# Kernel tuning notes

Hardware: AMD Instinct MI355X
Metric: run time of the kernel (lower is better)

The kernel has to match this reference:

```python
import jax, jax.numpy as jnp
import numpy as np

EPS = 1e-5
GROUPS = 32

def group_norm(x, gamma, beta):
    B, C, H, W = x.shape
    g = x.reshape(B, GROUPS, C // GROUPS, H, W)
    mu = g.mean(axis=(2, 3, 4), keepdims=True)
    var = g.var(axis=(2, 3, 4), keepdims=True)
    g = (g - mu) * jax.lax.rsqrt(var + EPS)
    x = g.reshape(B, C, H, W)
    return x * gamma[None, :, None, None] + beta[None, :, None, None]

def setup_inputs() -> dict:
    key = jax.random.key(0)
    ks = jax.random.split(key, 6)
    C = 512
    x = jax.random.normal(ks[0], (16, C, 32, 32), dtype=jnp.float32)
    gamma = jnp.ones((C,), jnp.float32)
    beta = jnp.zeros((C,), jnp.float32)
    w_qkv = jax.random.normal(ks[1], (3 * C, C), jnp.float32) / np.sqrt(C)
    b_qkv = jnp.zeros((3 * C,), jnp.float32)
    w_proj = jax.random.normal(ks[2], (C, C), jnp.float32) / np.sqrt(C)
    b_proj = jnp.zeros((C,), jnp.float32)
    return {"x": x, "gamma": gamma, "beta": beta, "w_qkv": w_qkv,
            "b_qkv": b_qkv, "w_proj": w_proj, "b_proj": b_proj}

def reference(x, gamma, beta, w_qkv, b_qkv, w_proj, b_proj):
    B, C, H, W = x.shape
    h = group_norm(x, gamma, beta)
    # 1x1 conv == per-pixel linear over channels
    qkv = jnp.einsum('bchw,oc->bohw', h, w_qkv) + b_qkv[None, :, None, None]
    q, k, v = jnp.split(qkv, 3, axis=1)
    N = H * W
    q = q.reshape(B, C, N)            # [B,C,N]
    k = k.reshape(B, C, N)
    v = v.reshape(B, C, N)
    attn = jnp.einsum('bci,bcj->bij', q, k) / jnp.sqrt(jnp.float32(C))
    attn = jax.nn.softmax(attn, axis=-1)          # [B,N,N]
    out = jnp.einsum('bij,bcj->bci', attn, v)     # [B,C,N]
    out = out.reshape(B, C, H, W)
    out = jnp.einsum('bchw,oc->bohw', out, w_proj) + b_proj[None, :, None, None]
    return x + out
```

## Files before the change

kernel.cpp:

```cpp
#include <hip/hip_runtime.h>
#include <hip/hip_bf16.h>

#define BATCH 16
#define CH    512
#define NPIX  1024
#define GRP   32
#define CPG   16

typedef __attribute__((ext_vector_type(8))) short bf16x8;
typedef __attribute__((ext_vector_type(4))) float f32x4;

__device__ __forceinline__ ushort f2b(float f) {
    union { float f; unsigned u; } v; v.f = f;
    unsigned u = v.u;
    u += 0x7FFF + ((u >> 16) & 1);
    return (ushort)(u >> 16);
}

#define GLD16(gp, lp) __builtin_amdgcn_global_load_lds( \
    (__attribute__((address_space(1))) void*)(gp), \
    (__attribute__((address_space(3))) void*)(lp), 16, 0, 0)

__global__ __launch_bounds__(256) void convert_weights(
    const float* __restrict__ wq, const float* __restrict__ wp,
    ushort* __restrict__ wq_b, ushort* __restrict__ wp_b,
    float* __restrict__ rowsum) {
    int i = blockIdx.x * 256 + threadIdx.x;
    if (i < 786432) wq_b[i] = f2b(wq[i]);
    else            wp_b[i - 786432] = f2b(wp[i - 786432]);
    if (i < BATCH * NPIX) rowsum[i] = 0.f;
}

__global__ __launch_bounds__(256) void gn_fused(
    const float* __restrict__ x, const float* __restrict__ gamma,
    const float* __restrict__ beta, ushort* __restrict__ hT) {
    __shared__ float xs[CPG * NPIX];
    __shared__ float as[4], bs[4];
    int g = blockIdx.x, b = blockIdx.y;
    const float4* p = (const float4*)(x + ((size_t)b * CH + g * CPG) * NPIX);
    float4* xs4 = (float4*)xs;
    float s = 0.f, ss = 0.f;
    for (int i = threadIdx.x; i < 4096; i += 256) {
        float4 v = p[i];
        xs4[i] = v;
        s  += v.x + v.y + v.z + v.w;
        ss += v.x*v.x + v.y*v.y + v.z*v.z + v.w*v.w;
    }
    for (int o = 1; o < 64; o <<= 1) { s += __shfl_xor(s, o); ss += __shfl_xor(ss, o); }
    int w = threadIdx.x >> 6;
    if ((threadIdx.x & 63) == 0) { as[w] = s; bs[w] = ss; }
    __syncthreads();
    s  = as[0] + as[1] + as[2] + as[3];
    ss = bs[0] + bs[1] + bs[2] + bs[3];
    float m   = s * (1.0f / 16384.0f);
    float var = ss * (1.0f / 16384.0f) - m * m;
    float r   = rsqrtf(var + 1e-5f);

    int c0 = g * CPG;
    float ga[CPG], be[CPG];
#pragma unroll
    for (int c = 0; c < CPG; c++) {
        float gg = gamma[c0 + c] * r;
        ga[c] = gg;
        be[c] = beta[c0 + c] - m * gg;
    }
    ushort tmp[CPG];
#pragma unroll
    for (int i = 0; i < 4; i++) {
        int n = threadIdx.x + i * 256;
#pragma unroll
        for (int c = 0; c < CPG; c++)
            tmp[c] = f2b(xs[c * NPIX + n] * ga[c] + be[c]);
        uint4* dst = (uint4*)(hT + ((size_t)b * NPIX + n) * CH + c0);
        dst[0] = *(const uint4*)&tmp[0];
        dst[1] = *(const uint4*)&tmp[8];
    }
}

#define BK 64

template<int EPI, int BMt, int BNt>
__global__ __launch_bounds__(256, 4) void gemm_bt(
    const ushort* __restrict__ A, long sA, int lda,
    const ushort* __restrict__ Bt, long sB, int ldb,
    int K,
    void* __restrict__ Out, long sO, int ldo,
    const float* __restrict__ bias,
    const float* __restrict__ resid,
    ushort* __restrict__ vout,
    float* __restrict__ rowsum,
    float scale) {
    constexpr int FM = BMt / 32;
    constexpr int FN = BNt / 32;
    constexpr int SA = BMt / 32;
    constexpr int SB = BNt / 32;
    __shared__ __align__(16) ushort sh[(BMt + BNt) * BK];
    ushort* As = sh;
    ushort* Bs = sh + BMt * BK;

    int nx = gridDim.x, ny = gridDim.y;
    int L = blockIdx.x + nx * (blockIdx.y + ny * blockIdx.z);
    int per = (nx * ny * (int)gridDim.z) >> 3;
    int wid = (L & 7) * per + (L >> 3);
    int bx = wid % nx; wid /= nx;
    int by = wid % ny;
    int b  = wid / ny;

    A  += (size_t)b * sA;
    Bt += (size_t)b * sB;
    int m0 = by * BMt, n0 = bx * BNt;
    int tid = threadIdx.x;
    int lane = tid & 63;
    int wave = tid >> 6;
    int q = lane >> 4, l = lane & 15;
    int wm = (wave >> 1) * (BMt / 2), wn = (wave & 1) * (BNt / 2);

    int aoff[SA], boff[SB], lofa[SA], lofb[SB];
#pragma unroll
    for (int i = 0; i < SA; i++) {
        int p = tid + i * 256, r = p >> 3, g = (p & 7) ^ (r & 7);
        aoff[i] = (m0 + r) * lda + g * 8;
        lofa[i] = p * 8;
    }
#pragma unroll
    for (int i = 0; i < SB; i++) {
        int p = tid + i * 256, r = p >> 3, g = (p & 7) ^ (r & 7);
        boff[i] = (n0 + r) * ldb + g * 8;
        lofb[i] = p * 8;
    }

    int offA[FM][2], offB[FN][2];
#pragma unroll
    for (int mi = 0; mi < FM; mi++) {
        int r = wm + mi * 16 + l;
#pragma unroll
        for (int kk = 0; kk < 2; kk++)
            offA[mi][kk] = r * 64 + ((((kk << 2) | q) ^ (r & 7)) * 8);
    }
#pragma unroll
    for (int ni = 0; ni < FN; ni++) {
        int r = wn + ni * 16 + l;
#pragma unroll
        for (int kk = 0; kk < 2; kk++)
            offB[ni][kk] = r * 64 + ((((kk << 2) | q) ^ (r & 7)) * 8);
    }

    f32x4 zero = {0.f, 0.f, 0.f, 0.f};
    f32x4 acc[FM][FN];
#pragma unroll
    for (int mi = 0; mi < FM; mi++)
#pragma unroll
        for (int ni = 0; ni < FN; ni++) acc[mi][ni] = zero;

    for (int k0 = 0; k0 < K; k0 += BK) {
        __syncthreads();
#pragma unroll
        for (int i = 0; i < SA; i++) GLD16(A + aoff[i] + k0, As + lofa[i]);
#pragma unroll
        for (int i = 0; i < SB; i++) GLD16(Bt + boff[i] + k0, Bs + lofb[i]);
        __syncthreads();
#pragma unroll
        for (int kk = 0; kk < 2; kk++) {
            bf16x8 af[FM], bfr[FN];
#pragma unroll
            for (int mi = 0; mi < FM; mi++) af[mi]  = *(const bf16x8*)(As + offA[mi][kk]);
#pragma unroll
            for (int ni = 0; ni < FN; ni++) bfr[ni] = *(const bf16x8*)(Bs + offB[ni][kk]);
#pragma unroll
            for (int mi = 0; mi < FM; mi++)
#pragma unroll
                for (int ni = 0; ni < FN; ni++)
                    acc[mi][ni] = __builtin_amdgcn_mfma_f32_16x16x32_bf16(
                        af[mi], bfr[ni], acc[mi][ni], 0, 0, 0);
        }
    }

    if (EPI == 0) {
        if (n0 >= 1024) {
            __syncthreads();
#pragma unroll
            for (int mi = 0; mi < FM; mi++)
#pragma unroll
                for (int ni = 0; ni < FN; ni++) {
                    int nl = wn + ni * 16 + l;
                    float bi = bias[n0 + nl];
#pragma unroll
                    for (int rg = 0; rg < 4; rg++) {
                        int ml = wm + mi * 16 + q * 4 + rg;
                        int pos = (ml >> 3) ^ (nl & 15);
                        sh[nl * 128 + pos * 8 + (ml & 7)] = f2b(acc[mi][ni][rg] + bi);
                    }
                }
            __syncthreads();
#pragma unroll
            for (int i = 0; i < 8; i++) {
                int idx = tid + i * 256;
                int nl = idx >> 4, ch = idx & 15;
                int g2 = ch ^ (nl & 15);
                uint4 val = *(const uint4*)&sh[nl * 128 + g2 * 8];
                *(uint4*)(vout + (size_t)b * (512 * 1024)
                          + (size_t)(n0 - 1024 + nl) * 1024 + m0 + ch * 8) = val;
            }
            return;
        }
#pragma unroll
        for (int mi = 0; mi < FM; mi++)
#pragma unroll
            for (int ni = 0; ni < FN; ni++) {
                int n = n0 + wn + ni * 16 + l;
                float bi = bias[n];
#pragma unroll
                for (int rg = 0; rg < 4; rg++) {
                    int m = m0 + wm + mi * 16 + q * 4 + rg;
                    ((ushort*)Out)[(size_t)b * sO + (size_t)m * ldo + n] =
                        f2b(acc[mi][ni][rg] + bi);
                }
            }
        return;
    }
    if (EPI == 1) {
#pragma unroll
        for (int mi = 0; mi < FM; mi++) {
            float rsum[4] = {0.f, 0.f, 0.f, 0.f};
#pragma unroll
            for (int ni = 0; ni < FN; ni++) {
                int n = n0 + wn + ni * 16 + l;
#pragma unroll
                for (int rg = 0; rg < 4; rg++) {
                    int m = m0 + wm + mi * 16 + q * 4 + rg;
                    float u = __expf(acc[mi][ni][rg] * scale);
                    rsum[rg] += u;
                    ((ushort*)Out)[(size_t)b * sO + (size_t)m * ldo + n] = f2b(u);
                }
            }
#pragma unroll
            for (int rg = 0; rg < 4; rg++) {
                float s = rsum[rg];
                s += __shfl_xor(s, 1); s += __shfl_xor(s, 2);
                s += __shfl_xor(s, 4); s += __shfl_xor(s, 8);
                if (l == 0)
                    atomicAdd(&rowsum[b * NPIX + m0 + wm + mi * 16 + q * 4 + rg], s);
            }
        }
        return;
    }
#pragma unroll
    for (int mi = 0; mi < FM; mi++) {
        float inv[4];
        if (EPI == 2) {
#pragma unroll
            for (int rg = 0; rg < 4; rg++)
                inv[rg] = 1.0f / rowsum[b * NPIX + m0 + wm + mi * 16 + q * 4 + rg];
        }
#pragma unroll
        for (int ni = 0; ni < FN; ni++) {
            int mbase = m0 + wm + mi * 16 + q * 4;
            int n = n0 + wn + ni * 16 + l;
#pragma unroll
            for (int rg = 0; rg < 4; rg++) {
                int m = mbase + rg;
                float v = acc[mi][ni][rg];
                if (EPI == 2) {
                    ((ushort*)Out)[(size_t)b * sO + (size_t)m * ldo + n] = f2b(v * inv[rg]);
                } else {
                    v += bias[m] + resid[(size_t)b * sO + (size_t)m * ldo + n];
                    ((float*)Out)[(size_t)b * sO + (size_t)m * ldo + n] = v;
                }
            }
        }
    }
}

extern "C" void kernel_launch(void* const* d_in, const int* in_sizes, int n_in,
                              void* d_out, int out_size, void* d_ws, size_t ws_size,
                              hipStream_t stream) {
    const float* x     = (const float*)d_in[0];
    const float* gamma = (const float*)d_in[1];
    const float* beta  = (const float*)d_in[2];
    const float* wqkv  = (const float*)d_in[3];
    const float* bqkv  = (const float*)d_in[4];
    const float* wproj = (const float*)d_in[5];
    const float* bproj = (const float*)d_in[6];
    float* out = (float*)d_out;
    char* ws = (char*)d_ws;

    ushort* wq_b   = (ushort*)(ws + 0);
    ushort* wp_b   = (ushort*)(ws + 1572864);
    float*  rowsum = (float*)(ws + 2101248);
    ushort* hT     = (ushort*)(ws + 2166784);
    ushort* qk     = (ushort*)(ws + 18944000);
    ushort* vb     = (ushort*)(ws + 52498432);
    ushort* u      = (ushort*)(ws + 69275648);
    ushort* O1T    = hT;

    convert_weights<<<4096, 256, 0, stream>>>(wqkv, wproj, wq_b, wp_b, rowsum);
    gn_fused<<<dim3(GRP, BATCH), 256, 0, stream>>>(x, gamma, beta, hT);

    gemm_bt<0, 128, 128><<<dim3(12, 8, BATCH), 256, 0, stream>>>(
        hT, 524288, 512, wq_b, 0, 512, 512,
        qk, 1048576, 1024, bqkv, nullptr, vb, nullptr, 0.f);

    gemm_bt<1, 128, 128><<<dim3(8, 8, BATCH), 256, 0, stream>>>(
        qk, 1048576, 1024, qk + 512, 1048576, 1024, 512,
        u, 1048576, 1024, nullptr, nullptr, nullptr, rowsum, 0.044194173824159216f);

    gemm_bt<2, 128, 64><<<dim3(8, 8, BATCH), 256, 0, stream>>>(
        u, 1048576, 1024, vb, 524288, 1024, 1024,
        O1T, 524288, 512, nullptr, nullptr, nullptr, rowsum, 0.f);

    gemm_bt<3, 64, 128><<<dim3(8, 8, BATCH), 256, 0, stream>>>(
        wp_b, 0, 512, O1T, 524288, 512, 512,
        out, 524288, 1024, bproj, x, nullptr, nullptr, 0.f);
}
```

Baseline: 211.8 us.

## Double-buffer LDS tiles in gemm_bt to overlap global loads with MFMA

Doubles the shared-memory tile buffer and prefetches the next K-slice via global_load_lds while the current slice is consumed by MFMAs, using explicit vmcnt waits and raw s_barrier instead of two __syncthreads per iteration. This is meant to hide global-memory latency behind compute. It doubles LDS usage, which may lower occupancy under the launch bound of 4 blocks per CU. Correctness also depends on the vmcnt counting matching exactly the issued loads.

Result: no change. 212.2 us (+0.2%).

```diff
diff --git a/kernel.cpp b/kernel.cpp
--- a/kernel.cpp
+++ b/kernel.cpp
@@ -94,9 +94,8 @@
     constexpr int FN = BNt / 32;
     constexpr int SA = BMt / 32;
     constexpr int SB = BNt / 32;
-    __shared__ __align__(16) ushort sh[(BMt + BNt) * BK];
-    ushort* As = sh;
-    ushort* Bs = sh + BMt * BK;
+    constexpr int BUFSZ = (BMt + BNt) * BK;
+    __shared__ __align__(16) ushort sh[2 * BUFSZ];
 
     int nx = gridDim.x, ny = gridDim.y;
     int L = blockIdx.x + nx * (blockIdx.y + ny * blockIdx.z);
@@ -152,20 +151,37 @@
 #pragma unroll
         for (int ni = 0; ni < FN; ni++) acc[mi][ni] = zero;
 
-    for (int k0 = 0; k0 < K; k0 += BK) {
-        __syncthreads();
-#pragma unroll
-        for (int i = 0; i < SA; i++) GLD16(A + aoff[i] + k0, As + lofa[i]);
-#pragma unroll
-        for (int i = 0; i < SB; i++) GLD16(Bt + boff[i] + k0, Bs + lofb[i]);
-        __syncthreads();
+#pragma unroll
+    for (int i = 0; i < SA; i++) GLD16(A + aoff[i], sh + lofa[i]);
+#pragma unroll
+    for (int i = 0; i < SB; i++) GLD16(Bt + boff[i], sh + BMt * BK + lofb[i]);
+
+    const int nt = K / BK;
+    for (int t = 0; t < nt; t++) {
+        const int cur = t & 1;
+        const ushort* Asc = sh + cur * BUFSZ;
+        const ushort* Bsc = Asc + BMt * BK;
+        if (t + 1 < nt) {
+            ushort* Asn = sh + (cur ^ 1) * BUFSZ;
+            ushort* Bsn = Asn + BMt * BK;
+            int k1 = (t + 1) * BK;
+#pragma unroll
+            for (int i = 0; i < SA; i++) GLD16(A + aoff[i] + k1, Asn + lofa[i]);
+#pragma unroll
+            for (int i = 0; i < SB; i++) GLD16(Bt + boff[i] + k1, Bsn + lofb[i]);
+            asm volatile("s_waitcnt vmcnt(%0)" :: "i"(SA + SB) : "memory");
+        } else {
+            asm volatile("s_waitcnt vmcnt(0)" ::: "memory");
+        }
+        __builtin_amdgcn_s_barrier();
+        __builtin_amdgcn_sched_barrier(0);
 #pragma unroll
         for (int kk = 0; kk < 2; kk++) {
             bf16x8 af[FM], bfr[FN];
 #pragma unroll
-            for (int mi = 0; mi < FM; mi++) af[mi]  = *(const bf16x8*)(As + offA[mi][kk]);
-#pragma unroll
-            for (int ni = 0; ni < FN; ni++) bfr[ni] = *(const bf16x8*)(Bs + offB[ni][kk]);
+            for (int mi = 0; mi < FM; mi++) af[mi]  = *(const bf16x8*)(Asc + offA[mi][kk]);
+#pragma unroll
+            for (int ni = 0; ni < FN; ni++) bfr[ni] = *(const bf16x8*)(Bsc + offB[ni][kk]);
 #pragma unroll
             for (int mi = 0; mi < FM; mi++)
 #pragma unroll
@@ -173,6 +189,8 @@
                     acc[mi][ni] = __builtin_amdgcn_mfma_f32_16x16x32_bf16(
                         af[mi], bfr[ni], acc[mi][ni], 0, 0, 0);
         }
+        __builtin_amdgcn_sched_barrier(0);
+        __builtin_amdgcn_s_barrier();
     }
 
     if (EPI == 0) {
```
